# Kernel optimization log

Measured on AMD Instinct MI355X. Metric: run time of the kernel, lower is better.

The kernel has to match this reference:

```python
import jax, jax.numpy as jnp
import numpy as np

B, L, D_MODEL = 8, 256, 256
D_STATE, D_INNER, DT_RANK, D_CONV = 16, 512, 16, 4


def _ln(x, g, b, eps):
    mu = x.mean(-1, keepdims=True)
    var = ((x - mu) ** 2).mean(-1, keepdims=True)
    return (x - mu) * jax.lax.rsqrt(var + eps) * g + b


def _ssm(x, W_in, conv_w, conv_b, W_x, W_dt, b_dt, A_log, Dp, W_out):
    # x: (B, L, D_MODEL) -- standard Mamba selective-scan block
    xz = x @ W_in                                  # (B,L,2*Di)
    xc, z = jnp.split(xz, 2, axis=-1)
    K = conv_w.shape[-1]
    xp = jnp.pad(xc, ((0, 0), (K - 1, 0), (0, 0)))  # causal depthwise conv
    xc = sum(xp[:, k:k + L, :] * conv_w[:, k] for k in range(K)) + conv_b
    xc = jax.nn.silu(xc)
    x_dbl = xc @ W_x                               # (B,L,R+2S)
    dt, Bm, Cm = jnp.split(x_dbl, [DT_RANK, DT_RANK + D_STATE], axis=-1)
    dt = jax.nn.softplus(dt @ W_dt + b_dt)         # (B,L,Di)
    A = -jnp.exp(A_log)                            # (Di,S)
    dA = jnp.exp(dt[..., None] * A)                # (B,L,Di,S)
    dBx = dt[..., None] * Bm[:, :, None, :] * xc[..., None]

    def step(h, inp):
        dA_t, dBx_t, C_t = inp
        h = dA_t * h + dBx_t                       # (B,Di,S)
        y = jnp.einsum('bds,bs->bd', h, C_t)
        return h, y

    h0 = jnp.zeros((xc.shape[0], D_INNER, D_STATE), xc.dtype)
    xs = (dA.transpose(1, 0, 2, 3), dBx.transpose(1, 0, 2, 3), Cm.transpose(1, 0, 2))
    _, ys = jax.lax.scan(step, h0, xs)             # (L,B,Di)
    y = ys.transpose(1, 0, 2) + xc * Dp
    y = y * jax.nn.silu(z)
    return y @ W_out


def _basic(x, ln_g, ln_b, ssm_params):
    # Basic_Block: ReLU(SSM(LN(x))) + x  (drop_path=0, attn_drop=0)
    return jax.nn.relu(_ssm(_ln(x, ln_g, ln_b, 1e-6), *ssm_params)) + x


def setup_inputs() -> dict:
    key = jax.random.key(0)
    ks = jax.random.split(key, 32)

    def n(k, shape, s=0.02):
        return jax.random.normal(k, shape, dtype=jnp.float32) * s

    inp = {}
    inp['x_spa'] = jax.random.normal(ks[0], (B, L, D_MODEL), dtype=jnp.float32)
    inp['x_spe'] = jax.random.normal(ks[1], (B, L, D_MODEL), dtype=jnp.float32)
    i = 2
    A_init = jnp.log(jnp.tile(jnp.arange(1, D_STATE + 1, dtype=jnp.float32), (D_INNER, 1)))
    for p in ('spa', 'spe'):
        inp[p + '_ln_g'] = jnp.ones((D_MODEL,), jnp.float32)
        inp[p + '_ln_b'] = jnp.zeros((D_MODEL,), jnp.float32)
        inp[p + '_W_in'] = n(ks[i], (D_MODEL, 2 * D_INNER)); i += 1
        inp[p + '_conv_w'] = n(ks[i], (D_INNER, D_CONV), 0.1); i += 1
        inp[p + '_conv_b'] = jnp.zeros((D_INNER,), jnp.float32)
        inp[p + '_W_x'] = n(ks[i], (D_INNER, DT_RANK + 2 * D_STATE)); i += 1
        inp[p + '_W_dt'] = n(ks[i], (DT_RANK, D_INNER), 0.1); i += 1
        inp[p + '_b_dt'] = n(ks[i], (D_INNER,), 0.1); i += 1
        inp[p + '_A_log'] = A_init
        inp[p + '_D'] = jnp.ones((D_INNER,), jnp.float32)
        inp[p + '_W_out'] = n(ks[i], (D_INNER, D_MODEL)); i += 1
    inp['sc_W'] = n(ks[i], (D_MODEL, D_MODEL)); i += 1
    inp['sc_b'] = jnp.zeros((D_MODEL,), jnp.float32)
    inp['sc_ln_g'] = jnp.ones((D_MODEL,), jnp.float32)
    inp['sc_ln_b'] = jnp.zeros((D_MODEL,), jnp.float32)
    inp['fusion_W'] = n(ks[i], (D_MODEL, D_MODEL))
    return inp


def reference(x_spa, x_spe,
              spa_ln_g, spa_ln_b, spa_W_in, spa_conv_w, spa_conv_b, spa_W_x,
              spa_W_dt, spa_b_dt, spa_A_log, spa_D, spa_W_out,
              spe_ln_g, spe_ln_b, spe_W_in, spe_conv_w, spe_conv_b, spe_W_x,
              spe_W_dt, spe_b_dt, spe_A_log, spe_D, spe_W_out,
              sc_W, sc_b, sc_ln_g, sc_ln_b, fusion_W):
    # shared shortcut: Linear + LayerNorm (eps=1e-5)
    ident_spa = _ln(x_spa @ sc_W + sc_b, sc_ln_g, sc_ln_b, 1e-5)
    ident_spe = _ln(x_spe @ sc_W + sc_b, sc_ln_g, sc_ln_b, 1e-5)
    spa_p = (spa_W_in, spa_conv_w, spa_conv_b, spa_W_x, spa_W_dt, spa_b_dt, spa_A_log, spa_D, spa_W_out)
    spe_p = (spe_W_in, spe_conv_w, spe_conv_b, spe_W_x, spe_W_dt, spe_b_dt, spe_A_log, spe_D, spe_W_out)
    a = _basic(x_spa, spa_ln_g, spa_ln_b, spa_p)
    e = _basic(x_spe, spe_ln_g, spe_ln_b, spe_p)
    # fusion gate: mean-pool both branches, Linear(no bias) + sigmoid, broadcast-mul
    fw = jax.nn.sigmoid(((a.mean(1) + e.mean(1)) * 0.5) @ fusion_W)[:, None, :]
    a = a * fw
    e = e * fw
    return (a + ident_spa, e + ident_spe)
```

## Files before the change

kernel.cpp:

```cpp
#include <hip/hip_runtime.h>
#include <hip/hip_bf16.h>
#include <math.h>

#define BD 8
#define LD 256
#define DM 256
#define DS 16
#define DI 512
#define RK 16

#define NROWS (2*BD*LD)
#define HALF_ROWS (BD*LD)

typedef __attribute__((ext_vector_type(8))) short bhalf8;
typedef __attribute__((ext_vector_type(4))) float f32x4;

__device__ __forceinline__ float siluf(float x){ return x / (1.f + __expf(-x)); }
__device__ __forceinline__ float softplusf(float x){
  return fmaxf(x, 0.f) + log1pf(__expf(-fabsf(x)));
}
__device__ __forceinline__ unsigned short f2bf(float f){
  __hip_bfloat16 h = __float2bfloat16(f);
  return *reinterpret_cast<unsigned short*>(&h);
}

__global__ __launch_bounds__(256) void k_transpose(
    const float* __restrict__ Wi_spa, const float* __restrict__ Wi_spe,
    const float* __restrict__ Wo_spa, const float* __restrict__ Wo_spe,
    const float* __restrict__ scW,
    const float* __restrict__ Wx_spa, const float* __restrict__ Wx_spe,
    unsigned short* __restrict__ Wt_i_spa, unsigned short* __restrict__ Wt_i_spe,
    unsigned short* __restrict__ Wt_o_spa, unsigned short* __restrict__ Wt_o_spe,
    unsigned short* __restrict__ scWt,
    unsigned short* __restrict__ Wxt_spa, unsigned short* __restrict__ Wxt_spe,
    float* __restrict__ pooled)
{
  __shared__ unsigned short tile[256][68];
  __shared__ float tile2[128][49];
  int b = blockIdx.x;
  int tid = threadIdx.x;
  if (b == 60){
    for (int i=tid; i<BD*DM; i+=256) pooled[i] = 0.f;
    return;
  }
  if (b >= 52){
    int bb = b - 52;
    int branch = bb >> 2, chunk = bb & 3;
    int k0 = chunk*128;
    const float* Wx = branch ? Wx_spe : Wx_spa;
    unsigned short* Wxt = branch ? Wxt_spe : Wxt_spa;
    for (int i=tid; i<128*48; i+=256){
      int kk = i/48, c = i - kk*48;
      tile2[kk][c] = Wx[(k0+kk)*48 + c];
    }
    __syncthreads();
    for (int i=tid; i<64*128; i+=256){
      int cc = i >> 7, kk = i & 127;
      float v = (cc < 48) ? tile2[kk][cc] : 0.f;
      Wxt[cc*512 + k0 + kk] = f2bf(v);
    }
    return;
  }
  const float* W; unsigned short* Wt; int N, K, c0, k0;
  if (b < 32){
    int bb = b & 15;
    W  = (b < 16) ? Wi_spa  : Wi_spe;
    Wt = (b < 16) ? Wt_i_spa: Wt_i_spe;
    N = 1024; K = 256; c0 = (bb >> 2)*256; k0 = (bb & 3)*64;
  } else if (b < 48){
    int bb = b - 32; int h = bb >> 3; bb &= 7;
    W  = h ? Wo_spe  : Wo_spa;
    Wt = h ? Wt_o_spe: Wt_o_spa;
    N = 256; K = 512; c0 = 0; k0 = bb*64;
  } else {
    int bb = b - 48;
    W = scW; Wt = scWt;
    N = 256; K = 256; c0 = 0; k0 = bb*64;
  }
  int c = c0 + tid;
  #pragma unroll 8
  for (int kk=0; kk<64; kk++)
    tile[tid][kk] = f2bf(W[(k0+kk)*N + c]);
  __syncthreads();
  for (int p=0; p<16; p++){
    int i = tid + 256*p;
    int cl = i >> 4, kq = (i & 15)*4;
    uint2 v = *(const uint2*)&tile[cl][kq];
    *(uint2*)&Wt[(c0+cl)*K + k0 + kq] = v;
  }
}

__global__ __launch_bounds__(256) void k_lnwin(
    const float* __restrict__ x_spa, const float* __restrict__ x_spe,
    const float* __restrict__ g_spa, const float* __restrict__ b_spa,
    const float* __restrict__ g_spe, const float* __restrict__ b_spe,
    const unsigned short* __restrict__ Wt_spa, const unsigned short* __restrict__ Wt_spe,
    float* __restrict__ xc_raw, float* __restrict__ szout)
{
  __shared__ unsigned short At[16][264];
  __shared__ float red[16][16];
  __shared__ float mu[16], rs[16];
  int tid = threadIdx.x;
  int bi = blockIdx.x;
  int rg = bi >> 2, cg = bi & 3;
  int r0 = rg * 16;
  int branch = (r0 >= HALF_ROWS);
  const float* xb = branch ? x_spe : x_spa;
  const float* g  = branch ? g_spe : g_spa;
  const float* be = branch ? b_spe : b_spa;
  const unsigned short* Wt = branch ? Wt_spe : Wt_spa;
  int rr0 = branch ? r0 - HALF_ROWS : r0;

  {
    int row = tid >> 4, seg = tid & 15;
    const float* xp = xb + (rr0 + row)*DM + seg*16;
    float s = 0.f;
    #pragma unroll
    for (int i=0;i<4;i++){
      float4 v = *(const float4*)(xp + i*4);
      s  += v.x+v.y+v.z+v.w;
    }
    red[row][seg] = s;
    __syncthreads();
    if (seg == 0){
      float t = 0.f;
      #pragma unroll
      for (int i=0;i<16;i++) t += red[row][i];
      mu[row] = t * (1.f/DM);
    }
    __syncthreads();
    float m = mu[row];
    float v2 = 0.f;
    #pragma unroll
    for (int i=0;i<4;i++){
      float4 v = *(const float4*)(xp + i*4);
      float dx=v.x-m, dy=v.y-m, dz=v.z-m, dw=v.w-m;
      v2 += dx*dx+dy*dy+dz*dz+dw*dw;
    }
    red[row][seg] = v2;
    __syncthreads();
    if (seg == 0){
      float t = 0.f;
      #pragma unroll
      for (int i=0;i<16;i++) t += red[row][i];
      rs[row] = rsqrtf(t*(1.f/DM) + 1e-6f);
    }
  }
  __syncthreads();
  for (int p=0;p<4;p++){
    int i4 = tid + 256*p;
    int r = i4 >> 6, kq = (i4 & 63)*4;
    float4 v  = *(const float4*)(xb + (rr0+r)*DM + kq);
    float4 gv = *(const float4*)(g + kq);
    float4 bv = *(const float4*)(be + kq);
    float m = mu[r], rv = rs[r];
    unsigned int lo = (unsigned int)f2bf((v.x-m)*rv*gv.x + bv.x)
                    | ((unsigned int)f2bf((v.y-m)*rv*gv.y + bv.y) << 16);
    unsigned int hi = (unsigned int)f2bf((v.z-m)*rv*gv.z + bv.z)
                    | ((unsigned int)f2bf((v.w-m)*rv*gv.w + bv.w) << 16);
    *(uint2*)&At[r][kq] = make_uint2(lo, hi);
  }
  __syncthreads();
  int w = tid >> 6, lane = tid & 63;
  int m16 = lane & 15, quad = lane >> 4;
  bhalf8 af[8];
  #pragma unroll
  for (int ks=0; ks<8; ks++)
    af[ks] = *(const bhalf8*)&At[m16][ks*32 + quad*8];
  f32x4 acc[4];
  #pragma unroll
  for (int ct=0; ct<4; ct++) acc[ct] = (f32x4)(0.f);
  const unsigned short* Wbw = Wt + (cg*256 + w*64)*256;
  #pragma unroll
  for (int ks=0; ks<8; ks++){
    #pragma unroll
    for (int ct=0; ct<4; ct++){
      bhalf8 bf = *(const bhalf8*)&Wbw[(ct*16 + m16)*256 + ks*32 + quad*8];
      acc[ct] = __builtin_amdgcn_mfma_f32_16x16x32_bf16(af[ks], bf, acc[ct], 0,0,0);
    }
  }
  bool isz = (cg >= 2);
  float* outp = isz ? szout : xc_raw;
  int cbase = (cg & 1)*256 + w*64;
  #pragma unroll
  for (int ct=0; ct<4; ct++){
    #pragma unroll
    for (int e=0;e<4;e++){
      int row = r0 + quad*4 + e;
      int col = cbase + ct*16 + m16;
      float v = acc[ct][e];
      if (isz) v = siluf(v);
      outp[row*DI + col] = v;
    }
  }
}

__global__ __launch_bounds__(256) void k_shortcut(
    const float* __restrict__ x_spa, const float* __restrict__ x_spe,
    const unsigned short* __restrict__ scWt, const float* __restrict__ sc_b,
    const float* __restrict__ ln_g, const float* __restrict__ ln_b,
    float* __restrict__ ident)
{
  __shared__ unsigned short At[16][264];
  __shared__ float Dt[16][260];
  __shared__ float red[16][16];
  __shared__ float mu[16], rs[16];
  int tid = threadIdx.x;
  int r0 = blockIdx.x * 16;
  int branch = (r0 >= HALF_ROWS);
  const float* xb = branch ? x_spe : x_spa;
  int rr0 = branch ? r0 - HALF_ROWS : r0;
  for (int p=0;p<4;p++){
    int i4 = tid + 256*p;
    int r = i4 >> 6, kq = (i4 & 63)*4;
    float4 v = *(const float4*)(xb + (rr0+r)*DM + kq);
    unsigned int lo = (unsigned int)f2bf(v.x) | ((unsigned int)f2bf(v.y) << 16);
    unsigned int hi = (unsigned int)f2bf(v.z) | ((unsigned int)f2bf(v.w) << 16);
    *(uint2*)&At[r][kq] = make_uint2(lo, hi);
  }
  __syncthreads();
  int w = tid >> 6, lane = tid & 63;
  int m16 = lane & 15, quad = lane >> 4;
  bhalf8 af[8];
  #pragma unroll
  for (int ks=0; ks<8; ks++)
    af[ks] = *(const bhalf8*)&At[m16][ks*32 + quad*8];
  f32x4 acc[4];
  #pragma unroll
  for (int ct=0; ct<4; ct++) acc[ct] = (f32x4)(0.f);
  const unsigned short* Wbw = scWt + (w*64)*256;
  #pragma unroll
  for (int ks=0; ks<8; ks++){
    #pragma unroll
    for (int ct=0; ct<4; ct++){
      bhalf8 bf = *(const bhalf8*)&Wbw[(ct*16 + m16)*256 + ks*32 + quad*8];
      acc[ct] = __builtin_amdgcn_mfma_f32_16x16x32_bf16(af[ks], bf, acc[ct], 0,0,0);
    }
  }
  #pragma unroll
  for (int ct=0; ct<4; ct++){
    #pragma unroll
    for (int e=0;e<4;e++){
      int row = quad*4 + e;
      int col = w*64 + ct*16 + m16;
      Dt[row][col] = acc[ct][e] + sc_b[col];
    }
  }
  __syncthreads();
  {
    int row = tid >> 4, seg = tid & 15;
    float s = 0.f, s2 = 0.f;
    #pragma unroll
    for (int i=0;i<4;i++){
      float4 v = *(const float4*)&Dt[row][seg*16 + i*4];
      s  += v.x+v.y+v.z+v.w;
      s2 += v.x*v.x + v.y*v.y + v.z*v.z + v.w*v.w;
    }
    red[row][seg] = s;
    __syncthreads();
    if (seg == 0){
      float t=0.f;
      #pragma unroll
      for (int i=0;i<16;i++) t += red[row][i];
      mu[row] = t * (1.f/DM);
    }
    __syncthreads();
    red[row][seg] = s2;
    __syncthreads();
    if (seg == 0){
      float t=0.f;
      #pragma unroll
      for (int i=0;i<16;i++) t += red[row][i];
      float m = mu[row];
      rs[row] = rsqrtf(t*(1.f/DM) - m*m + 1e-5f);
    }
  }
  __syncthreads();
  float gg = ln_g[tid], bb = ln_b[tid];
  #pragma unroll
  for (int r=0;r<16;r++)
    ident[(r0+r)*DM + tid] = (Dt[r][tid]-mu[r])*rs[r]*gg + bb;
}

__global__ __launch_bounds__(256) void k_convdbl(
    const float* __restrict__ cw_spa, const float* __restrict__ cb_spa,
    const float* __restrict__ cw_spe, const float* __restrict__ cb_spe,
    const float* __restrict__ xc_raw,
    const unsigned short* __restrict__ Wxt_spa, const unsigned short* __restrict__ Wxt_spe,
    const float* __restrict__ Wdt_spa, const float* __restrict__ bdt_spa,
    const float* __restrict__ Wdt_spe, const float* __restrict__ bdt_spe,
    float* __restrict__ xc, float* __restrict__ dt,
    float* __restrict__ Bm, float* __restrict__ Cm)
{
  __shared__ unsigned short At[16][520];
  __shared__ float xdbl[16][18];
  int tid = threadIdx.x;
  int r0 = blockIdx.x * 16;
  int branch = r0 >= HALF_ROWS;
  int l0 = r0 & (LD-1);
  const float* cw = branch ? cw_spe : cw_spa;
  const float* cb = branch ? cb_spe : cb_spa;
  const unsigned short* Wxt = branch ? Wxt_spe : Wxt_spa;
  const float* Wdt = branch ? Wdt_spe : Wdt_spa;
  const float* bdt = branch ? bdt_spe : bdt_spa;
  {
    int c = tid*2;
    float4 w0 = *(const float4*)(cw + 4*c);
    float4 w1 = *(const float4*)(cw + 4*(c+1));
    float2 bias = *(const float2*)(cb + c);
    float2 h0, h1, h2;
    if (l0 > 0){
      h0 = *(const float2*)(xc_raw + (r0-3)*DI + c);
      h1 = *(const float2*)(xc_raw + (r0-2)*DI + c);
      h2 = *(const float2*)(xc_raw + (r0-1)*DI + c);
    } else {
      h0 = make_float2(0.f,0.f); h1 = h0; h2 = h0;
    }
    #pragma unroll
    for (int r=0;r<16;r++){
      float2 cur = *(const float2*)(xc_raw + (r0+r)*DI + c);
      float vx = bias.x;
      vx = fmaf(h0.x, w0.x, vx); vx = fmaf(h1.x, w0.y, vx);
      vx = fmaf(h2.x, w0.z, vx); vx = fmaf(cur.x, w0.w, vx);
      float vy = bias.y;
      vy = fmaf(h0.y, w1.x, vy); vy = fmaf(h1.y, w1.y, vy);
      vy = fmaf(h2.y, w1.z, vy); vy = fmaf(cur.y, w1.w, vy);
      vx = siluf(vx); vy = siluf(vy);
      *(float2*)(xc + (r0+r)*DI + c) = make_float2(vx, vy);
      unsigned int pk = (unsigned int)f2bf(vx) | ((unsigned int)f2bf(vy) << 16);
      *(unsigned int*)&At[r][c] = pk;
      h0 = h1; h1 = h2; h2 = cur;
    }
  }
  __syncthreads();
  int w = tid >> 6, lane = tid & 63;
  int m16 = lane & 15, quad = lane >> 4;
  f32x4 acc = (f32x4)(0.f);
  #pragma unroll
  for (int ks=0; ks<16; ks++){
    bhalf8 a = *(const bhalf8*)&At[m16][ks*32 + quad*8];
    bhalf8 bf = *(const bhalf8*)&Wxt[(w*16 + m16)*512 + ks*32 + quad*8];
    acc = __builtin_amdgcn_mfma_f32_16x16x32_bf16(a, bf, acc, 0,0,0);
  }
  #pragma unroll
  for (int e=0;e<4;e++){
    int row = quad*4 + e;
    float v = acc[e];
    if (w == 0)      xdbl[row][m16] = v;
    else if (w == 1) Bm[(r0+row)*DS + m16] = v;
    else if (w == 2) Cm[(r0+row)*DS + m16] = v;
  }
  __syncthreads();
  float wdt0[16], wdt1[16];
  #pragma unroll
  for (int j=0;j<16;j++){ wdt0[j]=Wdt[j*DI+tid]; wdt1[j]=Wdt[j*DI+tid+256]; }
  float b0 = bdt[tid], b1 = bdt[tid+256];
  #pragma unroll
  for (int r=0;r<16;r++){
    float a0=b0, a1=b1;
    #pragma unroll
    for (int j=0;j<16;j++){
      float xv = xdbl[r][j];
      a0 = fmaf(xv, wdt0[j], a0);
      a1 = fmaf(xv, wdt1[j], a1);
    }
    dt[(r0+r)*DI + tid]       = softplusf(a0);
    dt[(r0+r)*DI + tid + 256] = softplusf(a1);
  }
}

__global__ __launch_bounds__(256) void k_scan(
    const float* __restrict__ Alog_spa, const float* __restrict__ Dp_spa,
    const float* __restrict__ Alog_spe, const float* __restrict__ Dp_spe,
    const float* __restrict__ dt, const float* __restrict__ xc,
    const float* __restrict__ sz, const float* __restrict__ Bm,
    const float* __restrict__ Cm, float* __restrict__ y)
{
  __shared__ float dts[16][20], xcs[16][20], szs[16][20], Bs[16][20], Cs[16][20];
  __shared__ float ypbuf[16][260];
  __shared__ float Dsh[16];
  int tid = threadIdx.x;
  int bi = blockIdx.x;
  int branch = bi >> 8;
  int rem = bi & 255;
  int b = rem >> 5;
  int d0 = (rem & 31) * 16;
  const float* Alog = branch ? Alog_spe : Alog_spa;
  const float* Dp   = branch ? Dp_spe   : Dp_spa;
  int dg = tid >> 4, s = tid & 15;
  int d = d0 + dg;
  float A_ds = -__expf(Alog[d*DS + s]);
  if (tid < 16) Dsh[tid] = Dp[d0 + tid];
  int row0 = branch*HALF_ROWS + b*LD;
  int rli = tid >> 4, rdd = tid & 15;
  float h = 0.f;
  for (int c=0; c<16; c++){
    int rbase = row0 + c*16;
    for (int idx=tid; idx<320; idx+=256){
      int arr = idx >> 6;
      int j = idx & 63;
      int r = j >> 2, c4 = (j & 3)*4;
      float4 v;
      if      (arr == 0) v = *(const float4*)(dt + (rbase+r)*DI + d0 + c4);
      else if (arr == 1) v = *(const float4*)(xc + (rbase+r)*DI + d0 + c4);
      else if (arr == 2) v = *(const float4*)(sz + (rbase+r)*DI + d0 + c4);
      else if (arr == 3) v = *(const float4*)(Bm + (rbase+r)*DS + c4);
      else               v = *(const float4*)(Cm + (rbase+r)*DS + c4);
      if      (arr == 0) *(float4*)&dts[r][c4] = v;
      else if (arr == 1) *(float4*)&xcs[r][c4] = v;
      else if (arr == 2) *(float4*)&szs[r][c4] = v;
      else if (arr == 3) *(float4*)&Bs[r][c4]  = v;
      else               *(float4*)&Cs[r][c4]  = v;
    }
    __syncthreads();
    #pragma unroll
    for (int li=0; li<16; li++){
      float dtv = dts[li][dg];
      float xcv = xcs[li][dg];
      float dA = __expf(dtv * A_ds);
      h = fmaf(dA, h, dtv * Bs[li][s] * xcv);
      ypbuf[li][s*16 + ((dg + s) & 15)] = h * Cs[li][s];
    }
    __syncthreads();
    float acc = 0.f;
    #pragma unroll
    for (int ss=0; ss<16; ss++)
      acc += ypbuf[rli][ss*16 + ((rdd + ss) & 15)];
    float xcv = xcs[rli][rdd];
    float szv = szs[rli][rdd];
    y[(rbase+rli)*DI + d0 + rdd] = fmaf(xcv, Dsh[rdd], acc) * szv;
    __syncthreads();
  }
}

__global__ __launch_bounds__(256) void k_wout(
    const unsigned short* __restrict__ Wt_spa, const unsigned short* __restrict__ Wt_spe,
    const float* __restrict__ x_spa, const float* __restrict__ x_spe,
    const float* __restrict__ y, float* __restrict__ ae,
    float* __restrict__ pooled)
{
  __shared__ unsigned short At[16][520];
  int tid = threadIdx.x;
  int bi = blockIdx.x;
  int r0 = (bi >> 1) * 16;
  int ch = bi & 1;
  int branch = (r0 >= HALF_ROWS);
  const unsigned short* Wt = branch ? Wt_spe : Wt_spa;
  const float* xb = branch ? x_spe : x_spa;
  int rr0 = branch ? r0 - HALF_ROWS : r0;
  for (int p=0;p<8;p++){
    int i4 = tid + 256*p;
    int r = i4 >> 7, kq = (i4 & 127)*4;
    float4 v = *(const float4*)(y + (r0+r)*DI + kq);
    unsigned int lo = (unsigned int)f2bf(v.x) | ((unsigned int)f2bf(v.y) << 16);
    unsigned int hi = (unsigned int)f2bf(v.z) | ((unsigned int)f2bf(v.w) << 16);
    *(uint2*)&At[r][kq] = make_uint2(lo, hi);
  }
  __syncthreads();
  int w = tid >> 6, lane = tid & 63;
  int m16 = lane & 15, quad = lane >> 4;
  bhalf8 af[16];
  #pragma unroll
  for (int ks=0; ks<16; ks++)
    af[ks] = *(const bhalf8*)&At[m16][ks*32 + quad*8];
  f32x4 acc[2];
  #pragma unroll
  for (int ct=0; ct<2; ct++) acc[ct] = (f32x4)(0.f);
  const unsigned short* Wbw = Wt + (ch*128 + w*32)*512;
  #pragma unroll
  for (int ks=0; ks<16; ks++){
    #pragma unroll
    for (int ct=0; ct<2; ct++){
      bhalf8 bf = *(const bhalf8*)&Wbw[(ct*16 + m16)*512 + ks*32 + quad*8];
      acc[ct] = __builtin_amdgcn_mfma_f32_16x16x32_bf16(af[ks], bf, acc[ct], 0,0,0);
    }
  }
  float ps0 = 0.f, ps1 = 0.f;
  #pragma unroll
  for (int ct=0; ct<2; ct++){
    #pragma unroll
    for (int e=0;e<4;e++){
      int row = quad*4 + e;
      int col = ch*128 + w*32 + ct*16 + m16;
      float v = fmaxf(acc[ct][e], 0.f) + xb[(rr0+row)*DM + col];
      ae[(r0+row)*DM + col] = v;
      if (ct == 0) ps0 += v; else ps1 += v;
    }
  }
  ps0 += __shfl_xor(ps0, 16, 64); ps0 += __shfl_xor(ps0, 32, 64);
  ps1 += __shfl_xor(ps1, 16, 64); ps1 += __shfl_xor(ps1, 32, 64);
  if (quad == 0){
    int bidx = (r0 >> 8) & 7;
    atomicAdd(&pooled[bidx*DM + ch*128 + w*32 + m16],      ps0);
    atomicAdd(&pooled[bidx*DM + ch*128 + w*32 + 16 + m16], ps1);
  }
}

__global__ __launch_bounds__(256) void k_gate(const float* __restrict__ pooled,
    const float* __restrict__ fW, float* __restrict__ fw)
{
  __shared__ float p[DM];
  int b=blockIdx.x, c=threadIdx.x;
  p[c] = pooled[b*DM+c] * (0.5f/LD);
  __syncthreads();
  float a=0.f;
  for(int k=0;k<DM;k+=4){
    a = fmaf(p[k+0], fW[(k+0)*DM+c], a);
    a = fmaf(p[k+1], fW[(k+1)*DM+c], a);
    a = fmaf(p[k+2], fW[(k+2)*DM+c], a);
    a = fmaf(p[k+3], fW[(k+3)*DM+c], a);
  }
  fw[b*DM+c]=1.f/(1.f+__expf(-a));
}

__global__ __launch_bounds__(256) void k_final(const float* __restrict__ ae,
    const float* __restrict__ ident, const float* __restrict__ fw, float* __restrict__ out)
{
  int idx4 = blockIdx.x*256 + threadIdx.x;
  int row = idx4 >> 6;
  int b = (row >> 8) & 7;
  int c4 = (idx4 & 63) * 4;
  float4 av = *(const float4*)(ae + idx4*4);
  float4 iv = *(const float4*)(ident + idx4*4);
  float4 fv = *(const float4*)(fw + b*DM + c4);
  float4 o;
  o.x = fmaf(av.x, fv.x, iv.x);
  o.y = fmaf(av.y, fv.y, iv.y);
  o.z = fmaf(av.z, fv.z, iv.z);
  o.w = fmaf(av.w, fv.w, iv.w);
  *(float4*)(out + idx4*4) = o;
}

extern "C" void kernel_launch(void* const* d_in, const int* in_sizes, int n_in,
                              void* d_out, int out_size, void* d_ws, size_t ws_size,
                              hipStream_t stream) {
  const float* x_spa     = (const float*)d_in[0];
  const float* x_spe     = (const float*)d_in[1];
  const float* spa_ln_g  = (const float*)d_in[2];
  const float* spa_ln_b  = (const float*)d_in[3];
  const float* spa_W_in  = (const float*)d_in[4];
  const float* spa_cw    = (const float*)d_in[5];
  const float* spa_cb    = (const float*)d_in[6];
  const float* spa_W_x   = (const float*)d_in[7];
  const float* spa_W_dt  = (const float*)d_in[8];
  const float* spa_b_dt  = (const float*)d_in[9];
  const float* spa_A_log = (const float*)d_in[10];
  const float* spa_D     = (const float*)d_in[11];
  const float* spa_W_out = (const float*)d_in[12];
  const float* spe_ln_g  = (const float*)d_in[13];
  const float* spe_ln_b  = (const float*)d_in[14];
  const float* spe_W_in  = (const float*)d_in[15];
  const float* spe_cw    = (const float*)d_in[16];
  const float* spe_cb    = (const float*)d_in[17];
  const float* spe_W_x   = (const float*)d_in[18];
  const float* spe_W_dt  = (const float*)d_in[19];
  const float* spe_b_dt  = (const float*)d_in[20];
  const float* spe_A_log = (const float*)d_in[21];
  const float* spe_D     = (const float*)d_in[22];
  const float* spe_W_out = (const float*)d_in[23];
  const float* sc_W      = (const float*)d_in[24];
  const float* sc_b      = (const float*)d_in[25];
  const float* sc_ln_g   = (const float*)d_in[26];
  const float* sc_ln_b   = (const float*)d_in[27];
  const float* fusion_W  = (const float*)d_in[28];

  float* ws = (float*)d_ws;
  float* ident  = ws;
  float* xc_raw = ident  + NROWS*DM;
  float* sz     = xc_raw + NROWS*DI;
  float* xc     = sz     + NROWS*DI;
  float* dt     = xc     + NROWS*DI;
  float* Bm     = dt     + NROWS*DI;
  float* Cm     = Bm     + NROWS*DS;
  float* pooled = Cm     + NROWS*DS;
  float* fw     = pooled + BD*DM;
  unsigned short* Wt_i_spa = (unsigned short*)(fw + BD*DM);
  unsigned short* Wt_i_spe = Wt_i_spa + 1024*256;
  unsigned short* Wt_o_spa = Wt_i_spe + 1024*256;
  unsigned short* Wt_o_spe = Wt_o_spa + 256*512;
  unsigned short* scWt     = Wt_o_spe + 256*512;
  unsigned short* Wxt_spa  = scWt     + 256*256;
  unsigned short* Wxt_spe  = Wxt_spa  + 64*512;

  float* out = (float*)d_out;

  k_transpose<<<61, 256, 0, stream>>>(spa_W_in, spe_W_in, spa_W_out, spe_W_out, sc_W,
                                      spa_W_x, spe_W_x,
                                      Wt_i_spa, Wt_i_spe, Wt_o_spa, Wt_o_spe, scWt,
                                      Wxt_spa, Wxt_spe, pooled);
  k_lnwin<<<1024, 256, 0, stream>>>(x_spa, x_spe, spa_ln_g, spa_ln_b, spe_ln_g, spe_ln_b,
                                    Wt_i_spa, Wt_i_spe, xc_raw, sz);
  k_convdbl<<<NROWS/16, 256, 0, stream>>>(spa_cw, spa_cb, spe_cw, spe_cb, xc_raw,
                                          Wxt_spa, Wxt_spe,
                                          spa_W_dt, spa_b_dt, spe_W_dt, spe_b_dt,
                                          xc, dt, Bm, Cm);
  float* y = xc_raw;
  k_scan<<<512, 256, 0, stream>>>(spa_A_log, spa_D, spe_A_log, spe_D, dt, xc, sz, Bm, Cm, y);
  k_shortcut<<<NROWS/16, 256, 0, stream>>>(x_spa, x_spe, scWt, sc_b, sc_ln_g, sc_ln_b, ident);
  float* ae = dt;
  k_wout<<<512, 256, 0, stream>>>(Wt_o_spa, Wt_o_spe, x_spa, x_spe, y, ae, pooled);
  k_gate<<<BD, 256, 0, stream>>>(pooled, fusion_W, fw);
  k_final<<<NROWS*DM/1024, 256, 0, stream>>>(ae, ident, fw, out);
}
```

Measured before the change: 215.3 us.

## Precompute LN'd bf16 activations in prep kernel and emit scan output as bf16

Moves the input LayerNorm and the bf16 conversion of x into the weight-prep kernel, using a one-pass mean/sumsq variance. k_lnwin previously recomputed the LN for each of its four column groups, so it and k_shortcut now just load bf16 rows. The scan kernel now keeps B/C/dt/xc in registers, reads xc/sz straight from global, and writes y as bf16, which halves the traffic into k_wout. In exchange, prep does more work and needs more shared memory, and the single-pass variance is slightly less numerically robust.

```diff
diff --git a/kernel.cpp b/kernel.cpp
--- a/kernel.cpp
+++ b/kernel.cpp
@@ -24,23 +24,90 @@
   return *reinterpret_cast<unsigned short*>(&h);
 }
 
-__global__ __launch_bounds__(256) void k_transpose(
+__global__ __launch_bounds__(256) void k_prep(
     const float* __restrict__ Wi_spa, const float* __restrict__ Wi_spe,
     const float* __restrict__ Wo_spa, const float* __restrict__ Wo_spe,
     const float* __restrict__ scW,
     const float* __restrict__ Wx_spa, const float* __restrict__ Wx_spe,
+    const float* __restrict__ x_spa, const float* __restrict__ x_spe,
+    const float* __restrict__ g_spa, const float* __restrict__ b_spa,
+    const float* __restrict__ g_spe, const float* __restrict__ b_spe,
     unsigned short* __restrict__ Wt_i_spa, unsigned short* __restrict__ Wt_i_spe,
     unsigned short* __restrict__ Wt_o_spa, unsigned short* __restrict__ Wt_o_spe,
     unsigned short* __restrict__ scWt,
     unsigned short* __restrict__ Wxt_spa, unsigned short* __restrict__ Wxt_spe,
+    unsigned short* __restrict__ xnbf, unsigned short* __restrict__ xbf,
     float* __restrict__ pooled)
 {
-  __shared__ unsigned short tile[256][68];
-  __shared__ float tile2[128][49];
+  __shared__ __align__(16) unsigned char smem[59904];
   int b = blockIdx.x;
   int tid = threadIdx.x;
   if (b == 60){
     for (int i=tid; i<BD*DM; i+=256) pooled[i] = 0.f;
+    return;
+  }
+  if (b >= 61){
+    float (*xst)[260] = (float (*)[260])smem;
+    float (*red)[16]  = (float (*)[16])(smem + 16640);
+    float *mu = (float*)(smem + 17664);
+    float *rs = (float*)(smem + 17728);
+    int r0g = (b - 61) * 16;
+    int branch = r0g >= HALF_ROWS;
+    const float* xb = branch ? x_spe : x_spa;
+    const float* g  = branch ? g_spe : g_spa;
+    const float* be = branch ? b_spe : b_spa;
+    int rr0 = branch ? r0g - HALF_ROWS : r0g;
+    for (int p=0;p<4;p++){
+      int i4 = tid + 256*p;
+      int r = i4 >> 6, c4 = (i4 & 63)*4;
+      *(float4*)&xst[r][c4] = *(const float4*)(xb + (rr0+r)*DM + c4);
+    }
+    __syncthreads();
+    {
+      int row = tid >> 4, seg = tid & 15;
+      float s = 0.f, s2 = 0.f;
+      #pragma unroll
+      for (int i=0;i<4;i++){
+        float4 v = *(float4*)&xst[row][seg*16 + i*4];
+        s  += v.x+v.y+v.z+v.w;
+        s2 += v.x*v.x + v.y*v.y + v.z*v.z + v.w*v.w;
+      }
+      red[row][seg] = s;
+      __syncthreads();
+      if (seg == 0){
+        float t=0.f;
+        #pragma unroll
+        for (int i=0;i<16;i++) t += red[row][i];
+        mu[row] = t * (1.f/DM);
+      }
+      __syncthreads();
+      red[row][seg] = s2;
+      __syncthreads();
+      if (seg == 0){
+        float t=0.f;
+        #pragma unroll
+        for (int i=0;i<16;i++) t += red[row][i];
+        float m = mu[row];
+        rs[row] = rsqrtf(t*(1.f/DM) - m*m + 1e-6f);
+      }
+    }
+    __syncthreads();
+    for (int p=0;p<4;p++){
+      int i4 = tid + 256*p;
+      int r = i4 >> 6, c4 = (i4 & 63)*4;
+      float4 v  = *(float4*)&xst[r][c4];
+      float4 gv = *(const float4*)(g + c4);
+      float4 bv = *(const float4*)(be + c4);
+      float m = mu[r], rv = rs[r];
+      unsigned int rlo = (unsigned int)f2bf(v.x) | ((unsigned int)f2bf(v.y) << 16);
+      unsigned int rhi = (unsigned int)f2bf(v.z) | ((unsigned int)f2bf(v.w) << 16);
+      *(uint2*)&xbf[(r0g+r)*DM + c4] = make_uint2(rlo, rhi);
+      unsigned int nlo = (unsigned int)f2bf((v.x-m)*rv*gv.x + bv.x)
+                       | ((unsigned int)f2bf((v.y-m)*rv*gv.y + bv.y) << 16);
+      unsigned int nhi = (unsigned int)f2bf((v.z-m)*rv*gv.z + bv.z)
+                       | ((unsigned int)f2bf((v.w-m)*rv*gv.w + bv.w) << 16);
+      *(uint2*)&xnbf[(r0g+r)*DM + c4] = make_uint2(nlo, nhi);
+    }
     return;
   }
   if (b >= 52){
@@ -49,6 +116,7 @@
     int k0 = chunk*128;
     const float* Wx = branch ? Wx_spe : Wx_spa;
     unsigned short* Wxt = branch ? Wxt_spe : Wxt_spa;
+    float (*tile2)[49] = (float (*)[49])(smem + 34816);
     for (int i=tid; i<128*48; i+=256){
       int kk = i/48, c = i - kk*48;
       tile2[kk][c] = Wx[(k0+kk)*48 + c];
@@ -61,6 +129,7 @@
     }
     return;
   }
+  unsigned short (*tile)[68] = (unsigned short (*)[68])smem;
   const float* W; unsigned short* Wt; int N, K, c0, k0;
   if (b < 32){
     int bb = b & 15;
@@ -91,74 +160,21 @@
 }
 
 __global__ __launch_bounds__(256) void k_lnwin(
-    const float* __restrict__ x_spa, const float* __restrict__ x_spe,
-    const float* __restrict__ g_spa, const float* __restrict__ b_spa,
-    const float* __restrict__ g_spe, const float* __restrict__ b_spe,
+    const unsigned short* __restrict__ xnbf,
     const unsigned short* __restrict__ Wt_spa, const unsigned short* __restrict__ Wt_spe,
     float* __restrict__ xc_raw, float* __restrict__ szout)
 {
   __shared__ unsigned short At[16][264];
-  __shared__ float red[16][16];
-  __shared__ float mu[16], rs[16];
   int tid = threadIdx.x;
   int bi = blockIdx.x;
   int rg = bi >> 2, cg = bi & 3;
   int r0 = rg * 16;
   int branch = (r0 >= HALF_ROWS);
-  const float* xb = branch ? x_spe : x_spa;
-  const float* g  = branch ? g_spe : g_spa;
-  const float* be = branch ? b_spe : b_spa;
   const unsigned short* Wt = branch ? Wt_spe : Wt_spa;
-  int rr0 = branch ? r0 - HALF_ROWS : r0;
-
-  {
-    int row = tid >> 4, seg = tid & 15;
-    const float* xp = xb + (rr0 + row)*DM + seg*16;
-    float s = 0.f;
-    #pragma unroll
-    for (int i=0;i<4;i++){
-      float4 v = *(const float4*)(xp + i*4);
-      s  += v.x+v.y+v.z+v.w;
-    }
-    red[row][seg] = s;
-    __syncthreads();
-    if (seg == 0){
-      float t = 0.f;
-      #pragma unroll
-      for (int i=0;i<16;i++) t += red[row][i];
-      mu[row] = t * (1.f/DM);
-    }
-    __syncthreads();
-    float m = mu[row];
-    float v2 = 0.f;
-    #pragma unroll
-    for (int i=0;i<4;i++){
-      float4 v = *(const float4*)(xp + i*4);
-      float dx=v.x-m, dy=v.y-m, dz=v.z-m, dw=v.w-m;
-      v2 += dx*dx+dy*dy+dz*dz+dw*dw;
-    }
-    red[row][seg] = v2;
-    __syncthreads();
-    if (seg == 0){
-      float t = 0.f;
-      #pragma unroll
-      for (int i=0;i<16;i++) t += red[row][i];
-      rs[row] = rsqrtf(t*(1.f/DM) + 1e-6f);
-    }
-  }
-  __syncthreads();
-  for (int p=0;p<4;p++){
-    int i4 = tid + 256*p;
-    int r = i4 >> 6, kq = (i4 & 63)*4;
-    float4 v  = *(const float4*)(xb + (rr0+r)*DM + kq);
-    float4 gv = *(const float4*)(g + kq);
-    float4 bv = *(const float4*)(be + kq);
-    float m = mu[r], rv = rs[r];
-    unsigned int lo = (unsigned int)f2bf((v.x-m)*rv*gv.x + bv.x)
-                    | ((unsigned int)f2bf((v.y-m)*rv*gv.y + bv.y) << 16);
-    unsigned int hi = (unsigned int)f2bf((v.z-m)*rv*gv.z + bv.z)
-                    | ((unsigned int)f2bf((v.w-m)*rv*gv.w + bv.w) << 16);
-    *(uint2*)&At[r][kq] = make_uint2(lo, hi);
+  for (int p=0;p<2;p++){
+    int i = tid + 256*p;
+    int r = i >> 5, oct = (i & 31)*8;
+    *(uint4*)&At[r][oct] = *(const uint4*)&xnbf[(r0+r)*DM + oct];
   }
   __syncthreads();
   int w = tid >> 6, lane = tid & 63;
@@ -196,7 +212,7 @@
 }
 
 __global__ __launch_bounds__(256) void k_shortcut(
-    const float* __restrict__ x_spa, const float* __restrict__ x_spe,
+    const unsigned short* __restrict__ xbf,
     const unsigned short* __restrict__ scWt, const float* __restrict__ sc_b,
     const float* __restrict__ ln_g, const float* __restrict__ ln_b,
     float* __restrict__ ident)
@@ -207,16 +223,10 @@
   __shared__ float mu[16], rs[16];
   int tid = threadIdx.x;
   int r0 = blockIdx.x * 16;
-  int branch = (r0 >= HALF_ROWS);
-  const float* xb = branch ? x_spe : x_spa;
-  int rr0 = branch ? r0 - HALF_ROWS : r0;
-  for (int p=0;p<4;p++){
-    int i4 = tid + 256*p;
-    int r = i4 >> 6, kq = (i4 & 63)*4;
-    float4 v = *(const float4*)(xb + (rr0+r)*DM + kq);
-    unsigned int lo = (unsigned int)f2bf(v.x) | ((unsigned int)f2bf(v.y) << 16);
-    unsigned int hi = (unsigned int)f2bf(v.z) | ((unsigned int)f2bf(v.w) << 16);
-    *(uint2*)&At[r][kq] = make_uint2(lo, hi);
+  for (int p=0;p<2;p++){
+    int i = tid + 256*p;
+    int r = i >> 5, oct = (i & 31)*8;
+    *(uint4*)&At[r][oct] = *(const uint4*)&xbf[(r0+r)*DM + oct];
   }
   __syncthreads();
   int w = tid >> 6, lane = tid & 63;
@@ -374,9 +384,9 @@
     const float* __restrict__ Alog_spe, const float* __restrict__ Dp_spe,
     const float* __restrict__ dt, const float* __restrict__ xc,
     const float* __restrict__ sz, const float* __restrict__ Bm,
-    const float* __restrict__ Cm, float* __restrict__ y)
-{
-  __shared__ float dts[16][20], xcs[16][20], szs[16][20], Bs[16][20], Cs[16][20];
+    const float* __restrict__ Cm, unsigned short* __restrict__ ybf)
+{
+  __shared__ float dts[16][20], xcs[16][20];
   __shared__ float ypbuf[16][260];
   __shared__ float Dsh[16];
   int tid = threadIdx.x;
@@ -392,43 +402,44 @@
   float A_ds = -__expf(Alog[d*DS + s]);
   if (tid < 16) Dsh[tid] = Dp[d0 + tid];
   int row0 = branch*HALF_ROWS + b*LD;
-  int rli = tid >> 4, rdd = tid & 15;
   float h = 0.f;
   for (int c=0; c<16; c++){
     int rbase = row0 + c*16;
-    for (int idx=tid; idx<320; idx+=256){
-      int arr = idx >> 6;
-      int j = idx & 63;
+    float rB[16], rC[16];
+    #pragma unroll
+    for (int li=0; li<16; li++){
+      rB[li] = Bm[(rbase+li)*DS + s];
+      rC[li] = Cm[(rbase+li)*DS + s];
+    }
+    if (tid < 128){
+      int arr = tid >> 6, j = tid & 63;
       int r = j >> 2, c4 = (j & 3)*4;
-      float4 v;
-      if      (arr == 0) v = *(const float4*)(dt + (rbase+r)*DI + d0 + c4);
-      else if (arr == 1) v = *(const float4*)(xc + (rbase+r)*DI + d0 + c4);
-      else if (arr == 2) v = *(const float4*)(sz + (rbase+r)*DI + d0 + c4);
-      else if (arr == 3) v = *(const float4*)(Bm + (rbase+r)*DS + c4);
-      else               v = *(const float4*)(Cm + (rbase+r)*DS + c4);
-      if      (arr == 0) *(float4*)&dts[r][c4] = v;
-      else if (arr == 1) *(float4*)&xcs[r][c4] = v;
-      else if (arr == 2) *(float4*)&szs[r][c4] = v;
-      else if (arr == 3) *(float4*)&Bs[r][c4]  = v;
-      else               *(float4*)&Cs[r][c4]  = v;
-    }
-    __syncthreads();
+      if (arr == 0) *(float4*)&dts[r][c4] = *(const float4*)(dt + (rbase+r)*DI + d0 + c4);
+      else          *(float4*)&xcs[r][c4] = *(const float4*)(xc + (rbase+r)*DI + d0 + c4);
+    }
+    __syncthreads();
+    float rdt[16], rxc[16];
+    #pragma unroll
+    for (int li=0; li<16; li++){ rdt[li] = dts[li][dg]; rxc[li] = xcs[li][dg]; }
+    float yp[16];
     #pragma unroll
     for (int li=0; li<16; li++){
-      float dtv = dts[li][dg];
-      float xcv = xcs[li][dg];
-      float dA = __expf(dtv * A_ds);
-      h = fmaf(dA, h, dtv * Bs[li][s] * xcv);
-      ypbuf[li][s*16 + ((dg + s) & 15)] = h * Cs[li][s];
-    }
+      float dA = __expf(rdt[li] * A_ds);
+      h = fmaf(dA, h, rdt[li] * rB[li] * rxc[li]);
+      yp[li] = h * rC[li];
+    }
+    #pragma unroll
+    for (int li=0; li<16; li++)
+      ypbuf[li][s*16 + ((dg + s) & 15)] = yp[li];
     __syncthreads();
     float acc = 0.f;
     #pragma unroll
     for (int ss=0; ss<16; ss++)
-      acc += ypbuf[rli][ss*16 + ((rdd + ss) & 15)];
-    float xcv = xcs[rli][rdd];
-    float szv = szs[rli][rdd];
-    y[(rbase+rli)*DI + d0 + rdd] = fmaf(xcv, Dsh[rdd], acc) * szv;
+      acc += ypbuf[dg][ss*16 + ((s + ss) & 15)];
+    float xcv = xc[(rbase+dg)*DI + d0 + s];
+    float szv = sz[(rbase+dg)*DI + d0 + s];
+    float yv = fmaf(xcv, Dsh[s], acc) * szv;
+    ybf[(rbase+dg)*DI + d0 + s] = f2bf(yv);
     __syncthreads();
   }
 }
@@ -436,7 +447,7 @@
 __global__ __launch_bounds__(256) void k_wout(
     const unsigned short* __restrict__ Wt_spa, const unsigned short* __restrict__ Wt_spe,
     const float* __restrict__ x_spa, const float* __restrict__ x_spe,
-    const float* __restrict__ y, float* __restrict__ ae,
+    const unsigned short* __restrict__ ybf, float* __restrict__ ae,
     float* __restrict__ pooled)
 {
   __shared__ unsigned short At[16][520];
@@ -448,13 +459,10 @@
   const unsigned short* Wt = branch ? Wt_spe : Wt_spa;
   const float* xb = branch ? x_spe : x_spa;
   int rr0 = branch ? r0 - HALF_ROWS : r0;
-  for (int p=0;p<8;p++){
-    int i4 = tid + 256*p;
-    int r = i4 >> 7, kq = (i4 & 127)*4;
-    float4 v = *(const float4*)(y + (r0+r)*DI + kq);
-    unsigned int lo = (unsigned int)f2bf(v.x) | ((unsigned int)f2bf(v.y) << 16);
-    unsigned int hi = (unsigned int)f2bf(v.z) | ((unsigned int)f2bf(v.w) << 16);
-    *(uint2*)&At[r][kq] = make_uint2(lo, hi);
+  for (int p=0;p<4;p++){
+    int i = tid + 256*p;
+    int r = i >> 6, oct = (i & 63)*8;
+    *(uint4*)&At[r][oct] = *(const uint4*)&ybf[(r0+r)*DI + oct];
   }
   __syncthreads();
   int w = tid >> 6, lane = tid & 63;
@@ -581,24 +589,26 @@
   unsigned short* scWt     = Wt_o_spe + 256*512;
   unsigned short* Wxt_spa  = scWt     + 256*256;
   unsigned short* Wxt_spe  = Wxt_spa  + 64*512;
+  unsigned short* xnbf     = Wxt_spe  + 64*512;
+  unsigned short* xbf      = xnbf     + NROWS*DM;
 
   float* out = (float*)d_out;
 
-  k_transpose<<<61, 256, 0, stream>>>(spa_W_in, spe_W_in, spa_W_out, spe_W_out, sc_W,
-                                      spa_W_x, spe_W_x,
-                                      Wt_i_spa, Wt_i_spe, Wt_o_spa, Wt_o_spe, scWt,
-                                      Wxt_spa, Wxt_spe, pooled);
-  k_lnwin<<<1024, 256, 0, stream>>>(x_spa, x_spe, spa_ln_g, spa_ln_b, spe_ln_g, spe_ln_b,
-                                    Wt_i_spa, Wt_i_spe, xc_raw, sz);
+  k_prep<<<317, 256, 0, stream>>>(spa_W_in, spe_W_in, spa_W_out, spe_W_out, sc_W,
+                                  spa_W_x, spe_W_x, x_spa, x_spe,
+                                  spa_ln_g, spa_ln_b, spe_ln_g, spe_ln_b,
+                                  Wt_i_spa, Wt_i_spe, Wt_o_spa, Wt_o_spe, scWt,
+                                  Wxt_spa, Wxt_spe, xnbf, xbf, pooled);
+  k_lnwin<<<1024, 256, 0, stream>>>(xnbf, Wt_i_spa, Wt_i_spe, xc_raw, sz);
   k_convdbl<<<NROWS/16, 256, 0, stream>>>(spa_cw, spa_cb, spe_cw, spe_cb, xc_raw,
                                           Wxt_spa, Wxt_spe,
                                           spa_W_dt, spa_b_dt, spe_W_dt, spe_b_dt,
                                           xc, dt, Bm, Cm);
-  float* y = xc_raw;
-  k_scan<<<512, 256, 0, stream>>>(spa_A_log, spa_D, spe_A_log, spe_D, dt, xc, sz, Bm, Cm, y);
-  k_shortcut<<<NROWS/16, 256, 0, stream>>>(x_spa, x_spe, scWt, sc_b, sc_ln_g, sc_ln_b, ident);
+  unsigned short* ybf = (unsigned short*)xc_raw;
+  k_scan<<<512, 256, 0, stream>>>(spa_A_log, spa_D, spe_A_log, spe_D, dt, xc, sz, Bm, Cm, ybf);
+  k_shortcut<<<NROWS/16, 256, 0, stream>>>(xbf, scWt, sc_b, sc_ln_g, sc_ln_b, ident);
   float* ae = dt;
-  k_wout<<<512, 256, 0, stream>>>(Wt_o_spa, Wt_o_spe, x_spa, x_spe, y, ae, pooled);
+  k_wout<<<512, 256, 0, stream>>>(Wt_o_spa, Wt_o_spe, x_spa, x_spe, ybf, ae, pooled);
   k_gate<<<BD, 256, 0, stream>>>(pooled, fusion_W, fw);
   k_final<<<NROWS*DM/1024, 256, 0, stream>>>(ae, ident, fw, out);
 }
```

Measured after the change: 210.4 us. -2.3%, faster.
